# Kernel optimization log

Hardware: AMD Instinct MI355X
Metric: run time of the kernel (lower is better)

The kernel has to match this reference:

```python
import jax, jax.numpy as jnp
import numpy as np

N_NODES = 50000


def _gcn_conv(x, edge_index, W, b):
    # x: [N, F_in], edge_index: [2, E] (with self-loops already added)
    n = x.shape[0]
    src, dst = edge_index[0], edge_index[1]
    h = x @ W  # [N, F_out] transform first (as in PyG GCNConv)
    deg = jax.ops.segment_sum(jnp.ones_like(dst, dtype=h.dtype), dst, num_segments=n)
    dinv = jax.lax.rsqrt(jnp.maximum(deg, 1.0))  # self-loops guarantee deg >= 1
    norm = dinv[src] * dinv[dst]  # [E]
    msg = h[src] * norm[:, None]  # [E, F_out] gather + scale
    out = jax.ops.segment_sum(msg, dst, num_segments=n)  # scatter-add to targets
    return out + b


def setup_inputs() -> dict:
    key = jax.random.key(0)
    k1, k2, k3, k4 = jax.random.split(key, 4)
    num_features, hidden, num_classes = 128, 128, 16
    n, e = N_NODES, 800000
    x = jax.random.normal(k1, (n, num_features), dtype=jnp.float32)
    edge_index = jax.random.randint(k2, (2, e), 0, n, dtype=jnp.int64)
    # add self-loops (PyG GCNConv default add_self_loops=True)
    loops = jnp.arange(n, dtype=jnp.int64)
    edge_index = jnp.concatenate([edge_index, jnp.stack([loops, loops])], axis=1)
    s1 = 1.0 / np.sqrt(num_features)
    s2 = 1.0 / np.sqrt(hidden)
    W1 = jax.random.uniform(k3, (num_features, hidden), jnp.float32, -s1, s1)
    b1 = jnp.zeros((hidden,), jnp.float32)
    W2 = jax.random.uniform(k4, (hidden, num_classes), jnp.float32, -s2, s2)
    b2 = jnp.zeros((num_classes,), jnp.float32)
    return {"x": x, "edge_index": edge_index, "W1": W1, "b1": b1, "W2": W2, "b2": b2}


def reference(x, edge_index, W1, b1, W2, b2):
    h = jax.nn.relu(_gcn_conv(x, edge_index, W1, b1))
    # dropout is identity in eval mode (deterministic reference)
    h = _gcn_conv(h, edge_index, W2, b2)
    return jax.nn.log_softmax(h, axis=1)
```

## Files before the change

### kernel.cpp

```cpp
#include <hip/hip_runtime.h>


typedef unsigned int uint32;
typedef unsigned short u16;
typedef __attribute__((ext_vector_type(8))) short bf16x8;
typedef __attribute__((ext_vector_type(4))) float f32x4;

#define NBMAX 1024
#define CHUNK 4096
#define EH 8192

__device__ inline u16 bf16rn(float f) {
    unsigned u = __float_as_uint(f);
    return (u16)((u + 0x7fffu + ((u >> 16) & 1u)) >> 16);
}

__device__ inline void bffma(float2& a, float w, uint32 u) {
    a.x = fmaf(w, __uint_as_float(u << 16), a.x);
    a.y = fmaf(w, __uint_as_float(u & 0xffff0000u), a.y);
}

__global__ __launch_bounds__(256) void k_combo(
    const float* __restrict__ x, const float* __restrict__ W1,
    const int* __restrict__ dstv, int* __restrict__ gh,
    u16* __restrict__ h, int N, int E, int NB, int ntile)
{
    __shared__ __align__(16) unsigned char smem[128 * 136 * 2];
    int t = threadIdx.x;

    if ((int)blockIdx.x >= ntile) {
        int* hl = (int*)smem;
        int hb = blockIdx.x - ntile;
        int e0 = hb * EH, e1 = min(e0 + EH, E);
        for (int i = t; i < NB; i += 256) hl[i] = 0;
        __syncthreads();
        for (int e = e0 + t; e < e1; e += 256)
            atomicAdd(&hl[dstv[e] >> 8], 1);
        __syncthreads();
        for (int i = t; i < NB; i += 256) {
            int c = hl[i];
            if (c) atomicAdd(&gh[i], c);
        }
        return;
    }

    u16* Wl = (u16*)smem;
    const float4* Wg4 = (const float4*)W1;
    for (int g = t; g < 128 * 32; g += 256) {
        int k = g >> 5, n4 = (g & 31) * 4;
        float4 v = Wg4[g];
        Wl[(n4 + 0) * 136 + k] = bf16rn(v.x);
        Wl[(n4 + 1) * 136 + k] = bf16rn(v.y);
        Wl[(n4 + 2) * 136 + k] = bf16rn(v.z);
        Wl[(n4 + 3) * 136 + k] = bf16rn(v.w);
    }
    __syncthreads();

    int wave = t >> 6, lane = t & 63;
    int quad = lane >> 4, ln = lane & 15;
    int rowbase = blockIdx.x * 64 + wave * 16;
    int node = rowbase + ln;
    int rclamp = min(node, N - 1);

    f32x4 acc[8];
    #pragma unroll
    for (int ct = 0; ct < 8; ++ct) acc[ct] = (f32x4){0.f, 0.f, 0.f, 0.f};

    #pragma unroll
    for (int q = 0; q < 4; ++q) {
        const float4* xr = (const float4*)(x + (size_t)rclamp * 128 + q * 32 + quad * 8);
        float4 a0 = xr[0], a1 = xr[1];
        bf16x8 xfr;
        xfr[0] = (short)bf16rn(a0.x); xfr[1] = (short)bf16rn(a0.y);
        xfr[2] = (short)bf16rn(a0.z); xfr[3] = (short)bf16rn(a0.w);
        xfr[4] = (short)bf16rn(a1.x); xfr[5] = (short)bf16rn(a1.y);
        xfr[6] = (short)bf16rn(a1.z); xfr[7] = (short)bf16rn(a1.w);
        #pragma unroll
        for (int ct = 0; ct < 8; ++ct) {
            bf16x8 wfr = *(const bf16x8*)&Wl[(ct * 16 + ln) * 136 + q * 32 + quad * 8];
            acc[ct] = __builtin_amdgcn_mfma_f32_16x16x32_bf16(wfr, xfr, acc[ct], 0, 0, 0);
        }
    }
    if (node < N) {
        u16* hp = h + (size_t)node * 128 + quad * 4;
        #pragma unroll
        for (int ct = 0; ct < 8; ++ct) {
            uint2 v;
            v.x = (uint32)bf16rn(acc[ct][0]) | ((uint32)bf16rn(acc[ct][1]) << 16);
            v.y = (uint32)bf16rn(acc[ct][2]) | ((uint32)bf16rn(acc[ct][3]) << 16);
            *(uint2*)(hp + ct * 16) = v;
        }
    }
}

__global__ __launch_bounds__(1024) void k_scanB(
    const int* __restrict__ gh, int* __restrict__ bbase,
    int* __restrict__ bfill, int NB, int E)
{
    __shared__ int s[1024];
    int t = threadIdx.x;
    int v = (t < NB) ? gh[t] : 0;
    s[t] = v;
    __syncthreads();
    for (int off = 1; off < 1024; off <<= 1) {
        int u = (t >= off) ? s[t - off] : 0;
        __syncthreads();
        s[t] += u;
        __syncthreads();
    }
    if (t < NB) {
        bbase[t] = s[t] - v;
        bfill[t] = 0;
    }
    if (t == 0) bbase[NB] = E;
}

__global__ __launch_bounds__(512) void k_partition(
    const int* __restrict__ src, const int* __restrict__ dstv,
    const int* __restrict__ bbase, int* __restrict__ bfill,
    uint32* __restrict__ tmp, int E, int NB)
{
    __shared__ int cntL[NBMAX];
    __shared__ int baseL[NBMAX];
    int t = threadIdx.x;
    int e0 = blockIdx.x * CHUNK;
    int e1 = min(e0 + CHUNK, E);
    for (int i = t; i < NB; i += 512) cntL[i] = 0;
    __syncthreads();
    for (int e = e0 + t; e < e1; e += 512)
        atomicAdd(&cntL[dstv[e] >> 8], 1);
    __syncthreads();
    for (int i = t; i < NB; i += 512) {
        int cc = cntL[i];
        baseL[i] = cc ? bbase[i] + atomicAdd(&bfill[i], cc) : 0;
        cntL[i] = 0;
    }
    __syncthreads();
    for (int e = e0 + t; e < e1; e += 512) {
        int sv = src[e], d = dstv[e];
        int b = d >> 8;
        int r = atomicAdd(&cntL[b], 1);
        tmp[baseL[b] + r] = (uint32)sv | ((uint32)(d & 255) << 16);
    }
}

__global__ __launch_bounds__(512) void k_bsort(
    const uint32* __restrict__ tmp, const int* __restrict__ bbase,
    u16* __restrict__ ssrc, int* __restrict__ rs,
    float* __restrict__ dinv, int N)
{
    __shared__ int cnt[256];
    __shared__ int ofs[256];
    int t = threadIdx.x;
    int b = blockIdx.x;
    int base = bbase[b];
    int endb = bbase[b + 1];
    int node0 = b << 8;

    if (t < 256) cnt[t] = 0;
    __syncthreads();
    for (int i = base + t; i < endb; i += 512)
        atomicAdd(&cnt[(tmp[i] >> 16) & 255], 1);
    __syncthreads();
    int v = (t < 256) ? cnt[t] : 0;
    __syncthreads();
    for (int off = 1; off < 256; off <<= 1) {
        int u = (t >= off && t < 256) ? cnt[t - off] : 0;
        __syncthreads();
        if (t < 256) cnt[t] += u;
        __syncthreads();
    }
    if (t < 256) {
        int node = node0 + t;
        if (node < N) {
            dinv[node] = rsqrtf(fmaxf((float)v, 1.0f));
            rs[node] = base + cnt[t];
        }
        ofs[t] = base + cnt[t] - v;
    }
    __syncthreads();
    for (int i = base + t; i < endb; i += 512) {
        uint32 rec = tmp[i];
        int pos = atomicAdd(&ofs[(rec >> 16) & 255], 1);
        ssrc[pos] = (u16)(rec & 0xffffu);
    }
}

__global__ __launch_bounds__(256) void k_pullg(
    const int* __restrict__ rs, const u16* __restrict__ ssrc,
    const float* __restrict__ dinv, const uint2* __restrict__ h,
    const float* __restrict__ b1, const float* __restrict__ W2,
    u16* __restrict__ h2, int N)
{
    __shared__ float W2T[16 * 132];
    __shared__ float rowbuf[8 * 132];
    int t = threadIdx.x;

    for (int g = t; g < 2048; g += 256) {
        int k = g >> 4, f = g & 15;
        W2T[f * 132 + k] = W2[g];
    }

    int wave = t >> 6, lane = t & 63;
    int sub = lane >> 5;
    int rl = lane & 31;
    int rowbase = blockIdx.x * 8;
    int n = rowbase + wave * 2 + sub;
    bool valid = (n < N);
    int nc = valid ? n : 0;
    int start = valid ? ((nc == 0) ? 0 : rs[nc - 1]) : 0;
    int len   = valid ? (rs[nc] - start) : 0;
    float dn  = valid ? dinv[nc] : 0.f;
    int lenMax = max(len, __shfl_xor(len, 32));

    float2 aA[4], aB[4];
    #pragma unroll
    for (int k = 0; k < 4; ++k) {
        aA[k] = (float2){0.f, 0.f};
        aB[k] = (float2){0.f, 0.f};
    }

    for (int tt = 0; tt < lenMax; tt += 4) {
        int s[4];
        uint2 u[4];
        float w[4];
        #pragma unroll
        for (int k = 0; k < 4; ++k) {
            bool act = (tt + k) < len;
            int jj = act ? (start + tt + k) : 0;
            s[k] = (int)ssrc[jj];
            w[k] = act ? 1.f : 0.f;
        }
        #pragma unroll
        for (int k = 0; k < 4; ++k)
            u[k] = h[(size_t)s[k] * 32 + rl];
        #pragma unroll
        for (int k = 0; k < 4; ++k)
            w[k] *= dn * dinv[s[k]];
        #pragma unroll
        for (int k = 0; k < 4; ++k) {
            bffma(aA[k], w[k], u[k].x);
            bffma(aB[k], w[k], u[k].y);
        }
    }

    {
        int r = wave * 2 + sub;
        float4 bb = ((const float4*)b1)[rl];
        float4 v;
        v.x = fmaxf(((aA[0].x + aA[1].x) + (aA[2].x + aA[3].x)) + bb.x, 0.f);
        v.y = fmaxf(((aA[0].y + aA[1].y) + (aA[2].y + aA[3].y)) + bb.y, 0.f);
        v.z = fmaxf(((aB[0].x + aB[1].x) + (aB[2].x + aB[3].x)) + bb.z, 0.f);
        v.w = fmaxf(((aB[0].y + aB[1].y) + (aB[2].y + aB[3].y)) + bb.w, 0.f);
        ((float4*)rowbuf)[r * 33 + rl] = v;
    }
    __syncthreads();

    if (t < 128) {
        int f = t & 15, r = t >> 4;
        const float4* W4 = (const float4*)W2T;
        const float4* rb4 = (const float4*)rowbuf;
        float acc = 0.f;
        #pragma unroll 8
        for (int k4 = 0; k4 < 32; ++k4) {
            float4 w = W4[f * 33 + k4];
            float4 xv = rb4[r * 33 + k4];
            acc = fmaf(xv.x, w.x, acc);
            acc = fmaf(xv.y, w.y, acc);
            acc = fmaf(xv.z, w.z, acc);
            acc = fmaf(xv.w, w.w, acc);
        }
        int rn = rowbase + r;
        if (rn < N) h2[(size_t)rn * 16 + f] = bf16rn(acc);
    }
}

__global__ __launch_bounds__(256) void k_pull2(
    const int* __restrict__ rs, const u16* __restrict__ ssrc,
    const float* __restrict__ dinv, const uint32* __restrict__ h2,
    const float* __restrict__ b2, float* __restrict__ out, int N)
{
    int idx = blockIdx.x * 256 + threadIdx.x;
    int n = idx >> 3;
    if (n >= N) return;
    int c = idx & 7;
    int start = (n == 0) ? 0 : rs[n - 1];
    int len = rs[n] - start;
    float dn = dinv[n];

    float2 a[4];
    #pragma unroll
    for (int k = 0; k < 4; ++k) a[k] = (float2){0.f, 0.f};

    for (int tt = 0; tt < len; tt += 4) {
        int s[4];
        uint32 u[4];
        float w[4];
        #pragma unroll
        for (int k = 0; k < 4; ++k) {
            bool act = (tt + k) < len;
            int jj = act ? (start + tt + k) : 0;
            s[k] = (int)ssrc[jj];
            w[k] = act ? 1.f : 0.f;
        }
        #pragma unroll
        for (int k = 0; k < 4; ++k)
            u[k] = h2[(size_t)s[k] * 8 + c];
        #pragma unroll
        for (int k = 0; k < 4; ++k)
            w[k] *= dn * dinv[s[k]];
        #pragma unroll
        for (int k = 0; k < 4; ++k)
            bffma(a[k], w[k], u[k]);
    }

    float acc0 = (a[0].x + a[1].x) + (a[2].x + a[3].x);
    float acc1 = (a[0].y + a[1].y) + (a[2].y + a[3].y);
    float v0 = acc0 + b2[2 * c];
    float v1 = acc1 + b2[2 * c + 1];
    float m = fmaxf(v0, v1);
    #pragma unroll
    for (int off = 1; off < 8; off <<= 1) m = fmaxf(m, __shfl_xor(m, off));
    float s = expf(v0 - m) + expf(v1 - m);
    #pragma unroll
    for (int off = 1; off < 8; off <<= 1) s += __shfl_xor(s, off);
    float ls = logf(s);
    float2 r = {v0 - m - ls, v1 - m - ls};
    ((float2*)out)[(size_t)n * 8 + c] = r;
}

extern "C" void kernel_launch(void* const* d_in, const int* in_sizes, int n_in,
                              void* d_out, int out_size, void* d_ws, size_t ws_size,
                              hipStream_t stream) {
    const float* x  = (const float*)d_in[0];
    const int*   ei = (const int*)d_in[1];
    const float* W1 = (const float*)d_in[2];
    const float* b1 = (const float*)d_in[3];
    const float* W2 = (const float*)d_in[4];
    const float* b2 = (const float*)d_in[5];
    float* outp = (float*)d_out;

    const int E = in_sizes[1] / 2;
    const int N = in_sizes[0] / 128;
    const int NB = (N + 255) >> 8;
    const int NH = (E + EH - 1) / EH;
    const int ntile = (N + 63) / 64;
    const int* src  = ei;
    const int* dstv = ei + E;

    const int Npad = (N + 255) & ~255;
    const int Epad = (E + 255) & ~255;
    int*   gh    = (int*)d_ws;
    int*   bbase = gh + NBMAX;
    int*   bfill = bbase + NBMAX + 256;
    int*   rs    = bfill + NBMAX;
    float* dinv  = (float*)(rs + Npad);
    uint32* tmp  = (uint32*)(dinv + Npad);
    u16*   ssrc  = (u16*)(tmp + Epad);
    uintptr_t hp = ((uintptr_t)(ssrc + Epad) + 255) & ~(uintptr_t)255;
    u16*   h     = (u16*)hp;
    u16*   h2    = h + (size_t)Npad * 128;

    hipMemsetAsync(gh, 0, NBMAX * sizeof(int), stream);
    k_combo<<<ntile + NH, 256, 0, stream>>>(x, W1, dstv, gh, h, N, E, NB, ntile);
    k_scanB<<<1, 1024, 0, stream>>>(gh, bbase, bfill, NB, E);
    k_partition<<<(E + CHUNK - 1) / CHUNK, 512, 0, stream>>>(src, dstv, bbase,
                                                             bfill, tmp, E, NB);
    k_bsort<<<NB, 512, 0, stream>>>(tmp, bbase, ssrc, rs, dinv, N);
    k_pullg<<<(N + 7) / 8, 256, 0, stream>>>(rs, ssrc, dinv, (const uint2*)h,
                                             b1, W2, h2, N);
    k_pull2<<<(N * 8 + 255) / 256, 256, 0, stream>>>(rs, ssrc, dinv,
                                                     (const uint32*)h2, b2, outp, N);
}
```

Before: 172.1 us.

## Pack bf16 source weights with edge indices and widen per-lane gather vectors

Adds a pass that packs each edge's source index with a bf16-rounded dinv[src] into one 32-bit record. Both aggregation kernels now read the weight from that record instead of doing a dependent gather of dinv[src], and they apply dn once after accumulation. The two pull kernels also widen per-lane loads: 16 bytes per lane with 4 rows per wave in layer 1, and 8 bytes per lane with 4 lanes per node in layer 2. This costs an extra kernel launch, doubles the size of the edge-index array, and lowers the precision of the normalisation weight to bf16.

```diff
diff --git a/kernel.cpp b/kernel.cpp
--- a/kernel.cpp
+++ b/kernel.cpp
@@ -146,7 +146,7 @@
 
 __global__ __launch_bounds__(512) void k_bsort(
     const uint32* __restrict__ tmp, const int* __restrict__ bbase,
-    u16* __restrict__ ssrc, int* __restrict__ rs,
+    uint32* __restrict__ srec, int* __restrict__ rs,
     float* __restrict__ dinv, int N)
 {
     __shared__ int cnt[256];
@@ -182,18 +182,27 @@
     for (int i = base + t; i < endb; i += 512) {
         uint32 rec = tmp[i];
         int pos = atomicAdd(&ofs[(rec >> 16) & 255], 1);
-        ssrc[pos] = (u16)(rec & 0xffffu);
-    }
+        srec[pos] = rec & 0xffffu;
+    }
+}
+
+__global__ __launch_bounds__(256) void k_wgt(
+    uint32* __restrict__ srec, const float* __restrict__ dinv, int E)
+{
+    int i = blockIdx.x * 256 + threadIdx.x;
+    if (i >= E) return;
+    uint32 s = srec[i] & 0xffffu;
+    srec[i] = s | ((uint32)bf16rn(dinv[s]) << 16);
 }
 
 __global__ __launch_bounds__(256) void k_pullg(
-    const int* __restrict__ rs, const u16* __restrict__ ssrc,
-    const float* __restrict__ dinv, const uint2* __restrict__ h,
+    const int* __restrict__ rs, const uint32* __restrict__ srec,
+    const float* __restrict__ dinv, const uint4* __restrict__ h4,
     const float* __restrict__ b1, const float* __restrict__ W2,
     u16* __restrict__ h2, int N)
 {
     __shared__ float W2T[16 * 132];
-    __shared__ float rowbuf[8 * 132];
+    __shared__ float rowbuf[16 * 132];
     int t = threadIdx.x;
 
     for (int g = t; g < 2048; g += 256) {
@@ -202,61 +211,70 @@
     }
 
     int wave = t >> 6, lane = t & 63;
-    int sub = lane >> 5;
-    int rl = lane & 31;
-    int rowbase = blockIdx.x * 8;
-    int n = rowbase + wave * 2 + sub;
+    int rr = lane >> 4;
+    int rl = lane & 15;
+    int rowbase = blockIdx.x * 16;
+    int n = rowbase + wave * 4 + rr;
     bool valid = (n < N);
     int nc = valid ? n : 0;
     int start = valid ? ((nc == 0) ? 0 : rs[nc - 1]) : 0;
     int len   = valid ? (rs[nc] - start) : 0;
     float dn  = valid ? dinv[nc] : 0.f;
-    int lenMax = max(len, __shfl_xor(len, 32));
-
-    float2 aA[4], aB[4];
+    int m = max(len, __shfl_xor(len, 16));
+    m = max(m, __shfl_xor(m, 32));
+
+    float2 aA[4], aB[4], aC[4], aD[4];
     #pragma unroll
     for (int k = 0; k < 4; ++k) {
-        aA[k] = (float2){0.f, 0.f};
-        aB[k] = (float2){0.f, 0.f};
-    }
-
-    for (int tt = 0; tt < lenMax; tt += 4) {
-        int s[4];
-        uint2 u[4];
+        aA[k] = (float2){0.f, 0.f}; aB[k] = (float2){0.f, 0.f};
+        aC[k] = (float2){0.f, 0.f}; aD[k] = (float2){0.f, 0.f};
+    }
+
+    for (int tt = 0; tt < m; tt += 4) {
+        uint32 rec[4];
+        uint4 u[4];
         float w[4];
         #pragma unroll
         for (int k = 0; k < 4; ++k) {
             bool act = (tt + k) < len;
             int jj = act ? (start + tt + k) : 0;
-            s[k] = (int)ssrc[jj];
+            rec[k] = srec[jj];
             w[k] = act ? 1.f : 0.f;
         }
         #pragma unroll
         for (int k = 0; k < 4; ++k)
-            u[k] = h[(size_t)s[k] * 32 + rl];
+            u[k] = h4[(size_t)(rec[k] & 0xffffu) * 16 + rl];
         #pragma unroll
         for (int k = 0; k < 4; ++k)
-            w[k] *= dn * dinv[s[k]];
+            w[k] *= __uint_as_float(rec[k] & 0xffff0000u);
         #pragma unroll
         for (int k = 0; k < 4; ++k) {
             bffma(aA[k], w[k], u[k].x);
             bffma(aB[k], w[k], u[k].y);
+            bffma(aC[k], w[k], u[k].z);
+            bffma(aD[k], w[k], u[k].w);
         }
     }
 
     {
-        int r = wave * 2 + sub;
-        float4 bb = ((const float4*)b1)[rl];
-        float4 v;
-        v.x = fmaxf(((aA[0].x + aA[1].x) + (aA[2].x + aA[3].x)) + bb.x, 0.f);
-        v.y = fmaxf(((aA[0].y + aA[1].y) + (aA[2].y + aA[3].y)) + bb.y, 0.f);
-        v.z = fmaxf(((aB[0].x + aB[1].x) + (aB[2].x + aB[3].x)) + bb.z, 0.f);
-        v.w = fmaxf(((aB[0].y + aB[1].y) + (aB[2].y + aB[3].y)) + bb.w, 0.f);
-        ((float4*)rowbuf)[r * 33 + rl] = v;
-    }
-    __syncthreads();
-
-    if (t < 128) {
+        int r = wave * 4 + rr;
+        float4 b0 = ((const float4*)b1)[rl * 2];
+        float4 b4 = ((const float4*)b1)[rl * 2 + 1];
+        float4 v0, v1;
+        v0.x = fmaxf(fmaf(dn, (aA[0].x + aA[1].x) + (aA[2].x + aA[3].x), b0.x), 0.f);
+        v0.y = fmaxf(fmaf(dn, (aA[0].y + aA[1].y) + (aA[2].y + aA[3].y), b0.y), 0.f);
+        v0.z = fmaxf(fmaf(dn, (aB[0].x + aB[1].x) + (aB[2].x + aB[3].x), b0.z), 0.f);
+        v0.w = fmaxf(fmaf(dn, (aB[0].y + aB[1].y) + (aB[2].y + aB[3].y), b0.w), 0.f);
+        v1.x = fmaxf(fmaf(dn, (aC[0].x + aC[1].x) + (aC[2].x + aC[3].x), b4.x), 0.f);
+        v1.y = fmaxf(fmaf(dn, (aC[0].y + aC[1].y) + (aC[2].y + aC[3].y), b4.y), 0.f);
+        v1.z = fmaxf(fmaf(dn, (aD[0].x + aD[1].x) + (aD[2].x + aD[3].x), b4.z), 0.f);
+        v1.w = fmaxf(fmaf(dn, (aD[0].y + aD[1].y) + (aD[2].y + aD[3].y), b4.w), 0.f);
+        ((float4*)rowbuf)[r * 33 + rl * 2] = v0;
+        ((float4*)rowbuf)[r * 33 + rl * 2 + 1] = v1;
+    }
+    __syncthreads();
+
+    {
         int f = t & 15, r = t >> 4;
         const float4* W4 = (const float4*)W2T;
         const float4* rb4 = (const float4*)rowbuf;
@@ -276,57 +294,63 @@
 }
 
 __global__ __launch_bounds__(256) void k_pull2(
-    const int* __restrict__ rs, const u16* __restrict__ ssrc,
-    const float* __restrict__ dinv, const uint32* __restrict__ h2,
+    const int* __restrict__ rs, const uint32* __restrict__ srec,
+    const float* __restrict__ dinv, const uint2* __restrict__ h2,
     const float* __restrict__ b2, float* __restrict__ out, int N)
 {
     int idx = blockIdx.x * 256 + threadIdx.x;
-    int n = idx >> 3;
+    int n = idx >> 2;
     if (n >= N) return;
-    int c = idx & 7;
+    int c4 = idx & 3;
     int start = (n == 0) ? 0 : rs[n - 1];
     int len = rs[n] - start;
     float dn = dinv[n];
 
-    float2 a[4];
+    float2 aX[4], aY[4];
     #pragma unroll
-    for (int k = 0; k < 4; ++k) a[k] = (float2){0.f, 0.f};
+    for (int k = 0; k < 4; ++k) {
+        aX[k] = (float2){0.f, 0.f};
+        aY[k] = (float2){0.f, 0.f};
+    }
 
     for (int tt = 0; tt < len; tt += 4) {
-        int s[4];
-        uint32 u[4];
+        uint32 rec[4];
+        uint2 u[4];
         float w[4];
         #pragma unroll
         for (int k = 0; k < 4; ++k) {
             bool act = (tt + k) < len;
             int jj = act ? (start + tt + k) : 0;
-            s[k] = (int)ssrc[jj];
+            rec[k] = srec[jj];
             w[k] = act ? 1.f : 0.f;
         }
         #pragma unroll
         for (int k = 0; k < 4; ++k)
-            u[k] = h2[(size_t)s[k] * 8 + c];
+            u[k] = h2[(size_t)(rec[k] & 0xffffu) * 4 + c4];
         #pragma unroll
         for (int k = 0; k < 4; ++k)
-            w[k] *= dn * dinv[s[k]];
-        #pragma unroll
-        for (int k = 0; k < 4; ++k)
-            bffma(a[k], w[k], u[k]);
-    }
-
-    float acc0 = (a[0].x + a[1].x) + (a[2].x + a[3].x);
-    float acc1 = (a[0].y + a[1].y) + (a[2].y + a[3].y);
-    float v0 = acc0 + b2[2 * c];
-    float v1 = acc1 + b2[2 * c + 1];
-    float m = fmaxf(v0, v1);
-    #pragma unroll
-    for (int off = 1; off < 8; off <<= 1) m = fmaxf(m, __shfl_xor(m, off));
-    float s = expf(v0 - m) + expf(v1 - m);
-    #pragma unroll
-    for (int off = 1; off < 8; off <<= 1) s += __shfl_xor(s, off);
+            w[k] *= __uint_as_float(rec[k] & 0xffff0000u);
+        #pragma unroll
+        for (int k = 0; k < 4; ++k) {
+            bffma(aX[k], w[k], u[k].x);
+            bffma(aY[k], w[k], u[k].y);
+        }
+    }
+
+    float4 bb = ((const float4*)b2)[c4];
+    float v0 = fmaf(dn, (aX[0].x + aX[1].x) + (aX[2].x + aX[3].x), bb.x);
+    float v1 = fmaf(dn, (aX[0].y + aX[1].y) + (aX[2].y + aX[3].y), bb.y);
+    float v2 = fmaf(dn, (aY[0].x + aY[1].x) + (aY[2].x + aY[3].x), bb.z);
+    float v3 = fmaf(dn, (aY[0].y + aY[1].y) + (aY[2].y + aY[3].y), bb.w);
+    float mx = fmaxf(fmaxf(v0, v1), fmaxf(v2, v3));
+    mx = fmaxf(mx, __shfl_xor(mx, 1));
+    mx = fmaxf(mx, __shfl_xor(mx, 2));
+    float s = expf(v0 - mx) + expf(v1 - mx) + expf(v2 - mx) + expf(v3 - mx);
+    s += __shfl_xor(s, 1);
+    s += __shfl_xor(s, 2);
     float ls = logf(s);
-    float2 r = {v0 - m - ls, v1 - m - ls};
-    ((float2*)out)[(size_t)n * 8 + c] = r;
+    float4 r = {v0 - mx - ls, v1 - mx - ls, v2 - mx - ls, v3 - mx - ls};
+    ((float4*)out)[(size_t)n * 4 + c4] = r;
 }
 
 extern "C" void kernel_launch(void* const* d_in, const int* in_sizes, int n_in,
@@ -356,8 +380,8 @@
     int*   rs    = bfill + NBMAX;
     float* dinv  = (float*)(rs + Npad);
     uint32* tmp  = (uint32*)(dinv + Npad);
-    u16*   ssrc  = (u16*)(tmp + Epad);
-    uintptr_t hp = ((uintptr_t)(ssrc + Epad) + 255) & ~(uintptr_t)255;
+    uint32* srec = tmp + Epad;
+    uintptr_t hp = ((uintptr_t)(srec + Epad) + 255) & ~(uintptr_t)255;
     u16*   h     = (u16*)hp;
     u16*   h2    = h + (size_t)Npad * 128;
 
@@ -366,9 +390,10 @@
     k_scanB<<<1, 1024, 0, stream>>>(gh, bbase, bfill, NB, E);
     k_partition<<<(E + CHUNK - 1) / CHUNK, 512, 0, stream>>>(src, dstv, bbase,
                                                              bfill, tmp, E, NB);
-    k_bsort<<<NB, 512, 0, stream>>>(tmp, bbase, ssrc, rs, dinv, N);
-    k_pullg<<<(N + 7) / 8, 256, 0, stream>>>(rs, ssrc, dinv, (const uint2*)h,
-                                             b1, W2, h2, N);
-    k_pull2<<<(N * 8 + 255) / 256, 256, 0, stream>>>(rs, ssrc, dinv,
-                                                     (const uint32*)h2, b2, outp, N);
-}
+    k_bsort<<<NB, 512, 0, stream>>>(tmp, bbase, srec, rs, dinv, N);
+    k_wgt<<<(E + 255) / 256, 256, 0, stream>>>(srec, dinv, E);
+    k_pullg<<<(N + 15) / 16, 256, 0, stream>>>(rs, srec, dinv, (const uint4*)h,
+                                               b1, W2, h2, N);
+    k_pull2<<<(N * 4 + 255) / 256, 256, 0, stream>>>(rs, srec, dinv,
+                                                     (const uint2*)h2, b2, outp, N);
+}
```

New measurement: 174.7 us. Within noise of the previous version (+1.5%).
